# Performance work log

Hardware: AMD Instinct MI355X
Metric: run time of the kernel (lower is better)

## Reference

```python
import jax, jax.numpy as jnp
import numpy as np

N_NODES = 50000
N_EDGES = 600000
CLASSIC_DIM = 128
GRAPH_OUTPUT_DIM = 96
NUM_RELATIONS = 4


def setup_inputs() -> dict:
    key = jax.random.key(0)
    ks = jax.random.split(key, 10)
    x = jax.random.normal(ks[0], (N_NODES, CLASSIC_DIM), dtype=jnp.float32)
    edge_index = jax.random.randint(ks[1], (2, N_EDGES), 0, N_NODES, dtype=jnp.int64)
    edge_type = jax.random.randint(ks[2], (N_EDGES,), 0, NUM_RELATIONS, dtype=jnp.int64)
    s1 = 1.0 / np.sqrt(CLASSIC_DIM)
    W_root1 = jax.random.normal(ks[3], (CLASSIC_DIM, CLASSIC_DIM), dtype=jnp.float32) * s1
    W_rel1 = jax.random.normal(ks[4], (NUM_RELATIONS, CLASSIC_DIM, CLASSIC_DIM), dtype=jnp.float32) * s1
    b1 = jnp.zeros((CLASSIC_DIM,), dtype=jnp.float32)
    W_root2 = jax.random.normal(ks[5], (CLASSIC_DIM, GRAPH_OUTPUT_DIM), dtype=jnp.float32) * s1
    W_rel2 = jax.random.normal(ks[6], (NUM_RELATIONS, CLASSIC_DIM, GRAPH_OUTPUT_DIM), dtype=jnp.float32) * s1
    b2 = jnp.zeros((GRAPH_OUTPUT_DIM,), dtype=jnp.float32)
    return {"classic_features": x, "edge_index": edge_index, "edge_type": edge_type,
            "W_root1": W_root1, "W_rel1": W_rel1, "b1": b1,
            "W_root2": W_root2, "W_rel2": W_rel2, "b2": b2}


def _rgcn_layer(x, edge_index, edge_type, W_root, W_rel, b):
    # RGCN: h_i = W_root x_i + b + sum_r (1/deg_{i,r}) * W_r * sum_{j in N_r(i)} x_j
    # Aggregate-then-transform (valid by linearity) to keep the matmul small.
    src, dst = edge_index[0], edge_index[1]
    msgs = x[src]  # [E, d_in] irregular gather
    out = x @ W_root + b
    n = x.shape[0]
    num_rel = W_rel.shape[0]
    for r in range(num_rel):  # small fixed loop over relation types
        mask = (edge_type == r).astype(x.dtype)  # [E]
        agg = jax.ops.segment_sum(msgs * mask[:, None], dst, num_segments=n)  # [N, d_in]
        deg = jax.ops.segment_sum(mask, dst, num_segments=n)  # [N]
        agg = agg / jnp.maximum(deg, 1.0)[:, None]  # mean per relation (PyG default norm)
        out = out + agg @ W_rel[r]
    return out


def reference(classic_features, edge_index, edge_type, W_root1, W_rel1, b1, W_root2, W_rel2, b2):
    h = _rgcn_layer(classic_features, edge_index, edge_type, W_root1, W_rel1, b1)
    h = jax.nn.relu(h)
    # dropout(0.2) is identity in eval mode
    out = _rgcn_layer(h, edge_index, edge_type, W_root2, W_rel2, b2)
    return out
```

## Files before the change

### kernel.cpp

```cpp
#include <hip/hip_runtime.h>

#define DIM_IN 128
#define NREL 4
#define KTOT (DIM_IN + NREL * DIM_IN)
#define CAP 32

typedef __attribute__((ext_vector_type(8))) short short8;
typedef __attribute__((ext_vector_type(4))) float floatx4;

__device__ inline unsigned short f2bf(float f) {
    union { float f; unsigned int i; } c;
    c.f = f;
    unsigned int r = c.i + 0x7FFF + ((c.i >> 16) & 1);
    return (unsigned short)(r >> 16);
}
__device__ inline float bf2f(unsigned short u) {
    union { unsigned int i; float f; } c;
    c.i = ((unsigned int)u) << 16;
    return c.f;
}

__device__ inline void gload16_lds(const void* g, void* l) {
    __builtin_amdgcn_global_load_lds((const __attribute__((address_space(1))) unsigned int*)g,
                                     (__attribute__((address_space(3))) unsigned int*)l,
                                     16, 0, 0);
}

__global__ __launch_bounds__(256) void prep_kernel(
    const float* __restrict__ x, unsigned short* __restrict__ xb, int n4,
    const float* __restrict__ Wroot1, const float* __restrict__ Wrel1,
    unsigned short* __restrict__ Wt1,
    const float* __restrict__ Wroot2, const float* __restrict__ Wrel2,
    unsigned short* __restrict__ Wt2,
    const int* __restrict__ ei, const int* __restrict__ et,
    int* __restrict__ counts, unsigned short* __restrict__ bucket, int E) {
    int t = blockIdx.x * 256 + threadIdx.x;
    if (t < E) {
        int b = ei[E + t] * NREL + et[t];
        int slot = atomicAdd(&counts[b], 1);
        if (slot < CAP) bucket[(size_t)b * CAP + slot] = (unsigned short)ei[t];
    }
    if (t < n4) {
        float4 v = ((const float4*)x)[t];
        ushort4 o;
        o.x = f2bf(v.x); o.y = f2bf(v.y); o.z = f2bf(v.z); o.w = f2bf(v.w);
        ((ushort4*)xb)[t] = o;
    }
    if (t < 128 * KTOT) {
        int n = t / KTOT, k = t - n * KTOT;
        float v = (k < DIM_IN) ? Wroot1[(size_t)k * 128 + n]
                               : Wrel1[(size_t)(k - DIM_IN) * 128 + n];
        Wt1[t] = f2bf(v);
    }
    if (t < 96 * KTOT) {
        int n = t / KTOT, k = t - n * KTOT;
        float v = (k < DIM_IN) ? Wroot2[(size_t)k * 96 + n]
                               : Wrel2[(size_t)(k - DIM_IN) * 96 + n];
        Wt2[t] = f2bf(v);
    }
}

__global__ __launch_bounds__(256) void agg_kernel(
    const unsigned short* __restrict__ feat, const unsigned short* __restrict__ bucket,
    const int* __restrict__ counts, unsigned short* __restrict__ agg, int nb) {
    int l16 = threadIdx.x & 15;
    int g = (blockIdx.x * 256 + threadIdx.x) >> 4;
    if (g >= nb) return;
    int cnt = counts[g];
    int m = (cnt < CAP) ? cnt : CAP;
    const unsigned short* bk = bucket + (size_t)g * CAP;
    const unsigned short* fb = feat + l16 * 8;
    float acc[8];
#pragma unroll
    for (int j = 0; j < 8; j++) acc[j] = 0.f;
    for (int base = 0; base < m; base += 16) {
        int mm = m - base;
        if (mm > 16) mm = 16;
        int pick = (l16 < mm) ? l16 : (mm - 1);
        int idx = bk[base + pick];
        int s0 = __shfl(idx, 0, 16);
        short8 u = *(const short8*)(fb + (size_t)s0 * DIM_IN);
        for (int j = 1; j < mm; j++) {
            int sn = __shfl(idx, j, 16);
            short8 un = *(const short8*)(fb + (size_t)sn * DIM_IN);
#pragma unroll
            for (int c = 0; c < 8; c++) acc[c] += bf2f((unsigned short)u[c]);
            u = un;
        }
#pragma unroll
        for (int c = 0; c < 8; c++) acc[c] += bf2f((unsigned short)u[c]);
    }
    float sc = (cnt > 0) ? (1.0f / (float)cnt) : 0.f;
    short8 o;
#pragma unroll
    for (int j = 0; j < 8; j++) o[j] = (short)f2bf(acc[j] * sc);
    *(short8*)(agg + (size_t)g * DIM_IN + l16 * 8) = o;
}

template <int NOUT, bool STORE_BF16_RELU>
__global__ __launch_bounds__(256) void mfma_gemm_kernel(
    const unsigned short* __restrict__ xb,
    const unsigned short* __restrict__ agg,
    const unsigned short* __restrict__ Wt,
    const float* __restrict__ bias,
    void* __restrict__ outp,
    int N) {
    constexpr int NT = NOUT / 32;
    constexpr int APAN = 64 * 32;
    constexpr int KS = KTOT / 64;
    __shared__ unsigned short sA[2][2 * APAN];
    const int t = threadIdx.x;
    const int w = t >> 6;
    const int lane = t & 63;
    const int q = lane >> 4;
    const int l15 = lane & 15;
    const int wm = w >> 1, wn = w & 1;
    const int m0 = blockIdx.x * 64;

    floatx4 acc[2][NT];
#pragma unroll
    for (int mt = 0; mt < 2; mt++)
#pragma unroll
        for (int nt = 0; nt < NT; nt++) acc[mt][nt] = (floatx4)0.f;

    const unsigned short* WtB = Wt + (size_t)(wn * (NOUT / 2) + l15) * KTOT + q * 8;

    auto stageA = [&](int ks, int buf) {
        const int k0 = ks * 64;
#pragma unroll
        for (int r = 0; r < 2; r++) {
            int idx = t + r * 256;
            int panel = idx >> 8;
            int rem = idx & 255;
            int row = rem >> 2, ch = rem & 3;
            int rowg = m0 + row;
            if (rowg >= N) rowg = N - 1;
            int col = panel * 32 + ch * 8;
            const unsigned short* gp =
                (k0 < DIM_IN)
                    ? (xb + (size_t)rowg * DIM_IN + k0 + col)
                    : (agg + (size_t)rowg * (NREL * DIM_IN) + (k0 - DIM_IN) + col);
            gload16_lds(gp, &sA[buf][(size_t)idx * 8]);
        }
    };

    stageA(0, 0);
    __syncthreads();
    for (int ks = 0; ks < KS; ks++) {
        const int cur = ks & 1;
        const int k0 = ks * 64;
        short8 bF[2][NT];
#pragma unroll
        for (int s = 0; s < 2; s++)
#pragma unroll
            for (int nt = 0; nt < NT; nt++)
                bF[s][nt] = *(const short8*)(WtB + (size_t)nt * 16 * KTOT + k0 + s * 32);
        if (ks + 1 < KS) stageA(ks + 1, cur ^ 1);
#pragma unroll
        for (int s = 0; s < 2; s++) {
            short8 aF[2];
#pragma unroll
            for (int mt = 0; mt < 2; mt++)
                aF[mt] = *(const short8*)(&sA[cur][(size_t)s * APAN +
                                                   (size_t)(wm * 32 + mt * 16 + l15) * 32 + q * 8]);
#pragma unroll
            for (int mt = 0; mt < 2; mt++)
#pragma unroll
                for (int nt = 0; nt < NT; nt++)
                    acc[mt][nt] = __builtin_amdgcn_mfma_f32_16x16x32_bf16(aF[mt], bF[s][nt],
                                                                          acc[mt][nt], 0, 0, 0);
        }
        __syncthreads();
    }

#pragma unroll
    for (int nt = 0; nt < NT; nt++) {
        int colg = wn * (NOUT / 2) + nt * 16 + l15;
        float bv = bias[colg];
#pragma unroll
        for (int mt = 0; mt < 2; mt++) {
            int rbase = m0 + wm * 32 + mt * 16 + q * 4;
#pragma unroll
            for (int r = 0; r < 4; r++) {
                int grow = rbase + r;
                if (grow < N) {
                    float v = acc[mt][nt][r] + bv;
                    if (STORE_BF16_RELU) {
                        v = fmaxf(v, 0.f);
                        ((unsigned short*)outp)[(size_t)grow * NOUT + colg] = f2bf(v);
                    } else {
                        ((float*)outp)[(size_t)grow * NOUT + colg] = v;
                    }
                }
            }
        }
    }
}

extern "C" void kernel_launch(void* const* d_in, const int* in_sizes, int n_in,
                              void* d_out, int out_size, void* d_ws, size_t ws_size,
                              hipStream_t stream) {
    const float* x = (const float*)d_in[0];
    const int* ei = (const int*)d_in[1];
    const int* et = (const int*)d_in[2];
    const float* Wroot1 = (const float*)d_in[3];
    const float* Wrel1 = (const float*)d_in[4];
    const float* b1 = (const float*)d_in[5];
    const float* Wroot2 = (const float*)d_in[6];
    const float* Wrel2 = (const float*)d_in[7];
    const float* b2 = (const float*)d_in[8];
    float* out = (float*)d_out;

    int N = in_sizes[0] / DIM_IN;
    int E = in_sizes[2];
    int nb = N * NREL;

    char* p = (char*)d_ws;
    unsigned short* xb = (unsigned short*)p;     p += (size_t)N * DIM_IN * 2;
    unsigned short* hb = (unsigned short*)p;     p += (size_t)N * DIM_IN * 2;
    unsigned short* agg = (unsigned short*)p;    p += (size_t)nb * DIM_IN * 2;
    unsigned short* Wt1 = (unsigned short*)p;    p += (size_t)128 * KTOT * 2;
    unsigned short* Wt2 = (unsigned short*)p;    p += (size_t)96 * KTOT * 2;
    int* counts = (int*)p;                       p += (size_t)nb * 4;
    unsigned short* bucket = (unsigned short*)p; p += (size_t)nb * CAP * 2;
    if ((size_t)(p - (char*)d_ws) > ws_size) return;

    int n4 = N * DIM_IN / 4;
    int prepWork = n4;
    if (prepWork < E) prepWork = E;
    if (prepWork < 128 * KTOT) prepWork = 128 * KTOT;

    hipMemsetAsync(counts, 0, (size_t)nb * sizeof(int), stream);
    prep_kernel<<<(prepWork + 255) / 256, 256, 0, stream>>>(
        x, xb, n4, Wroot1, Wrel1, Wt1, Wroot2, Wrel2, Wt2, ei, et, counts, bucket, E);

    int gAgg = (nb * 16 + 255) / 256;
    int gB = (N + 63) / 64;
    agg_kernel<<<gAgg, 256, 0, stream>>>(xb, bucket, counts, agg, nb);
    mfma_gemm_kernel<128, true><<<gB, 256, 0, stream>>>(xb, agg, Wt1, b1, hb, N);
    agg_kernel<<<gAgg, 256, 0, stream>>>(hb, bucket, counts, agg, nb);
    mfma_gemm_kernel<96, false><<<gB, 256, 0, stream>>>(hb, agg, Wt2, b2, out, N);
}
```

Baseline: 266.0 us.

## Fuse neighbor aggregation into GEMM kernel via LDS-resident aggregated tile

Merges the separate aggregation and MFMA GEMM kernels into one kernel per layer. Each 32-row block gathers its neighbors' features, writes the per-relation means straight into a swizzled LDS tile, then runs the GEMM over the full K dimension from LDS with register-prefetched weights. This removes the global agg buffer write and read plus two launches. The cost is smaller GEMM tiles (32 rows), larger LDS use that may lower occupancy, and a serialized gather-then-compute phase inside each block.

```diff
diff --git a/kernel.cpp b/kernel.cpp
--- a/kernel.cpp
+++ b/kernel.cpp
@@ -60,137 +60,140 @@
     }
 }
 
-__global__ __launch_bounds__(256) void agg_kernel(
-    const unsigned short* __restrict__ feat, const unsigned short* __restrict__ bucket,
-    const int* __restrict__ counts, unsigned short* __restrict__ agg, int nb) {
-    int l16 = threadIdx.x & 15;
-    int g = (blockIdx.x * 256 + threadIdx.x) >> 4;
-    if (g >= nb) return;
-    int cnt = counts[g];
-    int m = (cnt < CAP) ? cnt : CAP;
-    const unsigned short* bk = bucket + (size_t)g * CAP;
-    const unsigned short* fb = feat + l16 * 8;
-    float acc[8];
-#pragma unroll
-    for (int j = 0; j < 8; j++) acc[j] = 0.f;
-    for (int base = 0; base < m; base += 16) {
-        int mm = m - base;
-        if (mm > 16) mm = 16;
-        int pick = (l16 < mm) ? l16 : (mm - 1);
-        int idx = bk[base + pick];
-        int s0 = __shfl(idx, 0, 16);
-        short8 u = *(const short8*)(fb + (size_t)s0 * DIM_IN);
-        for (int j = 1; j < mm; j++) {
-            int sn = __shfl(idx, j, 16);
-            short8 un = *(const short8*)(fb + (size_t)sn * DIM_IN);
-#pragma unroll
-            for (int c = 0; c < 8; c++) acc[c] += bf2f((unsigned short)u[c]);
-            u = un;
-        }
-#pragma unroll
-        for (int c = 0; c < 8; c++) acc[c] += bf2f((unsigned short)u[c]);
-    }
-    float sc = (cnt > 0) ? (1.0f / (float)cnt) : 0.f;
-    short8 o;
-#pragma unroll
-    for (int j = 0; j < 8; j++) o[j] = (short)f2bf(acc[j] * sc);
-    *(short8*)(agg + (size_t)g * DIM_IN + l16 * 8) = o;
-}
-
 template <int NOUT, bool STORE_BF16_RELU>
-__global__ __launch_bounds__(256) void mfma_gemm_kernel(
-    const unsigned short* __restrict__ xb,
-    const unsigned short* __restrict__ agg,
+__global__ __launch_bounds__(256) void fused_layer_kernel(
+    const unsigned short* __restrict__ feat,
     const unsigned short* __restrict__ Wt,
     const float* __restrict__ bias,
+    const unsigned short* __restrict__ bucket,
+    const int* __restrict__ counts,
     void* __restrict__ outp,
     int N) {
     constexpr int NT = NOUT / 32;
-    constexpr int APAN = 64 * 32;
-    constexpr int KS = KTOT / 64;
-    __shared__ unsigned short sA[2][2 * APAN];
+    __shared__ unsigned short sA[20 * 32 * 32];
     const int t = threadIdx.x;
     const int w = t >> 6;
     const int lane = t & 63;
     const int q = lane >> 4;
     const int l15 = lane & 15;
+    const int m0 = blockIdx.x * 32;
+
+#pragma unroll
+    for (int i = 0; i < 2; i++) {
+        int slot = i * 256 + t;
+        int p = slot >> 7;
+        int rem = slot & 127;
+        int row = rem >> 2, qs = rem & 3;
+        int qq = qs ^ ((row >> 1) & 3);
+        int rowg = m0 + row;
+        if (rowg >= N) rowg = N - 1;
+        gload16_lds(feat + (size_t)rowg * DIM_IN + p * 32 + qq * 8, sA + (size_t)slot * 8);
+    }
+
+    {
+        int gi = t >> 4, l16 = t & 15;
+        int myBid = gi * 8 + (l16 & 7);
+        int myR = myBid >> 2, myJ = myBid & 3;
+        int myRowg = m0 + myR;
+        if (myRowg >= N) myRowg = N - 1;
+        int cv = counts[myRowg * NREL + myJ];
+        const unsigned short* fb = feat + l16 * 8;
+
+        for (int i = 0; i < 8; i++) {
+            int bid = gi * 8 + i;
+            int r = bid >> 2, j = bid & 3;
+            int rowg = m0 + r;
+            if (rowg >= N) rowg = N - 1;
+            int cnt = __shfl(cv, i, 16);
+            int m = (cnt < CAP) ? cnt : CAP;
+            const unsigned short* bk = bucket + (size_t)(rowg * NREL + j) * CAP;
+            float acc[8];
+#pragma unroll
+            for (int c = 0; c < 8; c++) acc[c] = 0.f;
+            for (int base = 0; base < m; base += 16) {
+                int mm = m - base;
+                if (mm > 16) mm = 16;
+                int pick = (l16 < mm) ? l16 : (mm - 1);
+                int idx = bk[base + pick];
+                int s0 = __shfl(idx, 0, 16);
+                short8 u = *(const short8*)(fb + (size_t)s0 * DIM_IN);
+                for (int jj = 1; jj < mm; jj++) {
+                    int sn = __shfl(idx, jj, 16);
+                    short8 un = *(const short8*)(fb + (size_t)sn * DIM_IN);
+#pragma unroll
+                    for (int c = 0; c < 8; c++) acc[c] += bf2f((unsigned short)u[c]);
+                    u = un;
+                }
+#pragma unroll
+                for (int c = 0; c < 8; c++) acc[c] += bf2f((unsigned short)u[c]);
+            }
+            float sc = (cnt > 0) ? (1.0f / (float)cnt) : 0.f;
+            short8 o;
+#pragma unroll
+            for (int c = 0; c < 8; c++) o[c] = (short)f2bf(acc[c] * sc);
+            int p = 4 + j * 4 + (l16 >> 2);
+            int qs = (l16 & 3) ^ ((r >> 1) & 3);
+            *(short8*)(sA + ((size_t)p * 32 + r) * 32 + qs * 8) = o;
+        }
+    }
+
+    __syncthreads();
+
     const int wm = w >> 1, wn = w & 1;
-    const int m0 = blockIdx.x * 64;
-
-    floatx4 acc[2][NT];
-#pragma unroll
-    for (int mt = 0; mt < 2; mt++)
-#pragma unroll
-        for (int nt = 0; nt < NT; nt++) acc[mt][nt] = (floatx4)0.f;
-
+    floatx4 acc[NT];
+#pragma unroll
+    for (int nt = 0; nt < NT; nt++) acc[nt] = (floatx4)0.f;
+
+    const int rowA = wm * 16 + l15;
+    const int qsA = q ^ ((l15 >> 1) & 3);
+    const unsigned short* sAp = sA + (size_t)rowA * 32 + (size_t)qsA * 8;
     const unsigned short* WtB = Wt + (size_t)(wn * (NOUT / 2) + l15) * KTOT + q * 8;
 
-    auto stageA = [&](int ks, int buf) {
-        const int k0 = ks * 64;
-#pragma unroll
-        for (int r = 0; r < 2; r++) {
-            int idx = t + r * 256;
-            int panel = idx >> 8;
-            int rem = idx & 255;
-            int row = rem >> 2, ch = rem & 3;
-            int rowg = m0 + row;
-            if (rowg >= N) rowg = N - 1;
-            int col = panel * 32 + ch * 8;
-            const unsigned short* gp =
-                (k0 < DIM_IN)
-                    ? (xb + (size_t)rowg * DIM_IN + k0 + col)
-                    : (agg + (size_t)rowg * (NREL * DIM_IN) + (k0 - DIM_IN) + col);
-            gload16_lds(gp, &sA[buf][(size_t)idx * 8]);
-        }
-    };
-
-    stageA(0, 0);
-    __syncthreads();
-    for (int ks = 0; ks < KS; ks++) {
-        const int cur = ks & 1;
-        const int k0 = ks * 64;
-        short8 bF[2][NT];
-#pragma unroll
-        for (int s = 0; s < 2; s++)
+    short8 b0[NT], b1[NT], b0n[NT], b1n[NT];
+#pragma unroll
+    for (int nt = 0; nt < NT; nt++) b0[nt] = *(const short8*)(WtB + (size_t)nt * 16 * KTOT);
+#pragma unroll
+    for (int nt = 0; nt < NT; nt++) b1[nt] = *(const short8*)(WtB + (size_t)nt * 16 * KTOT + 32);
+
+#pragma unroll
+    for (int kp = 0; kp < 10; kp++) {
+        if (kp < 9) {
 #pragma unroll
             for (int nt = 0; nt < NT; nt++)
-                bF[s][nt] = *(const short8*)(WtB + (size_t)nt * 16 * KTOT + k0 + s * 32);
-        if (ks + 1 < KS) stageA(ks + 1, cur ^ 1);
-#pragma unroll
-        for (int s = 0; s < 2; s++) {
-            short8 aF[2];
-#pragma unroll
-            for (int mt = 0; mt < 2; mt++)
-                aF[mt] = *(const short8*)(&sA[cur][(size_t)s * APAN +
-                                                   (size_t)(wm * 32 + mt * 16 + l15) * 32 + q * 8]);
-#pragma unroll
-            for (int mt = 0; mt < 2; mt++)
-#pragma unroll
-                for (int nt = 0; nt < NT; nt++)
-                    acc[mt][nt] = __builtin_amdgcn_mfma_f32_16x16x32_bf16(aF[mt], bF[s][nt],
-                                                                          acc[mt][nt], 0, 0, 0);
-        }
-        __syncthreads();
+                b0n[nt] = *(const short8*)(WtB + (size_t)nt * 16 * KTOT + (2 * kp + 2) * 32);
+        }
+        short8 a0 = *(const short8*)(sAp + (size_t)(2 * kp) * 1024);
+#pragma unroll
+        for (int nt = 0; nt < NT; nt++)
+            acc[nt] = __builtin_amdgcn_mfma_f32_16x16x32_bf16(a0, b0[nt], acc[nt], 0, 0, 0);
+        if (kp < 9) {
+#pragma unroll
+            for (int nt = 0; nt < NT; nt++)
+                b1n[nt] = *(const short8*)(WtB + (size_t)nt * 16 * KTOT + (2 * kp + 3) * 32);
+        }
+        short8 a1 = *(const short8*)(sAp + (size_t)(2 * kp + 1) * 1024);
+#pragma unroll
+        for (int nt = 0; nt < NT; nt++)
+            acc[nt] = __builtin_amdgcn_mfma_f32_16x16x32_bf16(a1, b1[nt], acc[nt], 0, 0, 0);
+#pragma unroll
+        for (int nt = 0; nt < NT; nt++) { b0[nt] = b0n[nt]; b1[nt] = b1n[nt]; }
     }
 
 #pragma unroll
     for (int nt = 0; nt < NT; nt++) {
         int colg = wn * (NOUT / 2) + nt * 16 + l15;
         float bv = bias[colg];
-#pragma unroll
-        for (int mt = 0; mt < 2; mt++) {
-            int rbase = m0 + wm * 32 + mt * 16 + q * 4;
-#pragma unroll
-            for (int r = 0; r < 4; r++) {
-                int grow = rbase + r;
-                if (grow < N) {
-                    float v = acc[mt][nt][r] + bv;
-                    if (STORE_BF16_RELU) {
-                        v = fmaxf(v, 0.f);
-                        ((unsigned short*)outp)[(size_t)grow * NOUT + colg] = f2bf(v);
-                    } else {
-                        ((float*)outp)[(size_t)grow * NOUT + colg] = v;
-                    }
+        int rbase = m0 + wm * 16 + q * 4;
+#pragma unroll
+        for (int r = 0; r < 4; r++) {
+            int grow = rbase + r;
+            if (grow < N) {
+                float v = acc[nt][r] + bv;
+                if (STORE_BF16_RELU) {
+                    v = fmaxf(v, 0.f);
+                    ((unsigned short*)outp)[(size_t)grow * NOUT + colg] = f2bf(v);
+                } else {
+                    ((float*)outp)[(size_t)grow * NOUT + colg] = v;
                 }
             }
         }
@@ -218,7 +221,6 @@
     char* p = (char*)d_ws;
     unsigned short* xb = (unsigned short*)p;     p += (size_t)N * DIM_IN * 2;
     unsigned short* hb = (unsigned short*)p;     p += (size_t)N * DIM_IN * 2;
-    unsigned short* agg = (unsigned short*)p;    p += (size_t)nb * DIM_IN * 2;
     unsigned short* Wt1 = (unsigned short*)p;    p += (size_t)128 * KTOT * 2;
     unsigned short* Wt2 = (unsigned short*)p;    p += (size_t)96 * KTOT * 2;
     int* counts = (int*)p;                       p += (size_t)nb * 4;
@@ -234,10 +236,7 @@
     prep_kernel<<<(prepWork + 255) / 256, 256, 0, stream>>>(
         x, xb, n4, Wroot1, Wrel1, Wt1, Wroot2, Wrel2, Wt2, ei, et, counts, bucket, E);
 
-    int gAgg = (nb * 16 + 255) / 256;
-    int gB = (N + 63) / 64;
-    agg_kernel<<<gAgg, 256, 0, stream>>>(xb, bucket, counts, agg, nb);
-    mfma_gemm_kernel<128, true><<<gB, 256, 0, stream>>>(xb, agg, Wt1, b1, hb, N);
-    agg_kernel<<<gAgg, 256, 0, stream>>>(hb, bucket, counts, agg, nb);
-    mfma_gemm_kernel<96, false><<<gB, 256, 0, stream>>>(hb, agg, Wt2, b2, out, N);
-}
+    int gF = (N + 31) / 32;
+    fused_layer_kernel<128, true><<<gF, 256, 0, stream>>>(xb, Wt1, b1, bucket, counts, hb, N);
+    fused_layer_kernel<96, false><<<gF, 256, 0, stream>>>(hb, Wt2, b2, bucket, counts, out, N);
+}
```

Measured after the change: 326.9 us. 22.9% more time.

## Load full 32-row A tile into LDS once and pipeline B fragments in registers

Applied to the files above, without the earlier changes.

The MFMA GEMM now uses 32-row blocks and stages the entire K=640 A tile into LDS in one pass with an XOR swizzle, instead of double-buffered 64-wide K steps with a sync per step. Weight fragments are prefetched four K-panels ahead in a register ring. This removes the per-step barriers, reduces LDS bank conflicts and doubles the grid size for more parallelism. In exchange it uses more LDS per block, loads weights twice as often per output row and gives each wave half as many MFMAs per A load.

```diff
diff --git a/kernel.cpp b/kernel.cpp
--- a/kernel.cpp
+++ b/kernel.cpp
@@ -106,91 +106,78 @@
     void* __restrict__ outp,
     int N) {
     constexpr int NT = NOUT / 32;
-    constexpr int APAN = 64 * 32;
-    constexpr int KS = KTOT / 64;
-    __shared__ unsigned short sA[2][2 * APAN];
+    __shared__ unsigned short sA[20 * 32 * 32];
     const int t = threadIdx.x;
     const int w = t >> 6;
     const int lane = t & 63;
     const int q = lane >> 4;
     const int l15 = lane & 15;
+    const int m0 = blockIdx.x * 32;
+
+#pragma unroll
+    for (int i = 0; i < 10; i++) {
+        int slot = i * 256 + t;
+        int p = slot >> 7;
+        int rem = slot & 127;
+        int row = rem >> 2, qs = rem & 3;
+        int qq = qs ^ ((row >> 1) & 3);
+        int rowg = m0 + row;
+        if (rowg >= N) rowg = N - 1;
+        const unsigned short* gp =
+            (p < 4) ? (xb + (size_t)rowg * DIM_IN + p * 32 + qq * 8)
+                    : (agg + (size_t)rowg * (NREL * DIM_IN) + (p - 4) * 32 + qq * 8);
+        gload16_lds(gp, sA + (size_t)slot * 8);
+    }
+    __syncthreads();
+
     const int wm = w >> 1, wn = w & 1;
-    const int m0 = blockIdx.x * 64;
-
-    floatx4 acc[2][NT];
-#pragma unroll
-    for (int mt = 0; mt < 2; mt++)
-#pragma unroll
-        for (int nt = 0; nt < NT; nt++) acc[mt][nt] = (floatx4)0.f;
-
+    floatx4 acc[NT];
+#pragma unroll
+    for (int nt = 0; nt < NT; nt++) acc[nt] = (floatx4)0.f;
+
+    const int rowA = wm * 16 + l15;
+    const int qsA = q ^ ((l15 >> 1) & 3);
+    const unsigned short* sAp = sA + (size_t)rowA * 32 + (size_t)qsA * 8;
     const unsigned short* WtB = Wt + (size_t)(wn * (NOUT / 2) + l15) * KTOT + q * 8;
 
-    auto stageA = [&](int ks, int buf) {
-        const int k0 = ks * 64;
-#pragma unroll
-        for (int r = 0; r < 2; r++) {
-            int idx = t + r * 256;
-            int panel = idx >> 8;
-            int rem = idx & 255;
-            int row = rem >> 2, ch = rem & 3;
-            int rowg = m0 + row;
-            if (rowg >= N) rowg = N - 1;
-            int col = panel * 32 + ch * 8;
-            const unsigned short* gp =
-                (k0 < DIM_IN)
-                    ? (xb + (size_t)rowg * DIM_IN + k0 + col)
-                    : (agg + (size_t)rowg * (NREL * DIM_IN) + (k0 - DIM_IN) + col);
-            gload16_lds(gp, &sA[buf][(size_t)idx * 8]);
+    short8 bf[4][NT];
+#pragma unroll
+    for (int d = 0; d < 4; d++)
+#pragma unroll
+        for (int nt = 0; nt < NT; nt++)
+            bf[d][nt] = *(const short8*)(WtB + (size_t)nt * 16 * KTOT + d * 32);
+
+#pragma unroll
+    for (int p = 0; p < 20; p++) {
+        short8 a = *(const short8*)(sAp + (size_t)p * 1024);
+        short8 cur[NT];
+#pragma unroll
+        for (int nt = 0; nt < NT; nt++) cur[nt] = bf[p & 3][nt];
+        if (p + 4 < 20) {
+#pragma unroll
+            for (int nt = 0; nt < NT; nt++)
+                bf[p & 3][nt] = *(const short8*)(WtB + (size_t)nt * 16 * KTOT + (p + 4) * 32);
         }
-    };
-
-    stageA(0, 0);
-    __syncthreads();
-    for (int ks = 0; ks < KS; ks++) {
-        const int cur = ks & 1;
-        const int k0 = ks * 64;
-        short8 bF[2][NT];
-#pragma unroll
-        for (int s = 0; s < 2; s++)
-#pragma unroll
-            for (int nt = 0; nt < NT; nt++)
-                bF[s][nt] = *(const short8*)(WtB + (size_t)nt * 16 * KTOT + k0 + s * 32);
-        if (ks + 1 < KS) stageA(ks + 1, cur ^ 1);
-#pragma unroll
-        for (int s = 0; s < 2; s++) {
-            short8 aF[2];
-#pragma unroll
-            for (int mt = 0; mt < 2; mt++)
-                aF[mt] = *(const short8*)(&sA[cur][(size_t)s * APAN +
-                                                   (size_t)(wm * 32 + mt * 16 + l15) * 32 + q * 8]);
-#pragma unroll
-            for (int mt = 0; mt < 2; mt++)
-#pragma unroll
-                for (int nt = 0; nt < NT; nt++)
-                    acc[mt][nt] = __builtin_amdgcn_mfma_f32_16x16x32_bf16(aF[mt], bF[s][nt],
-                                                                          acc[mt][nt], 0, 0, 0);
-        }
-        __syncthreads();
+#pragma unroll
+        for (int nt = 0; nt < NT; nt++)
+            acc[nt] = __builtin_amdgcn_mfma_f32_16x16x32_bf16(a, cur[nt], acc[nt], 0, 0, 0);
     }
 
 #pragma unroll
     for (int nt = 0; nt < NT; nt++) {
         int colg = wn * (NOUT / 2) + nt * 16 + l15;
         float bv = bias[colg];
-#pragma unroll
-        for (int mt = 0; mt < 2; mt++) {
-            int rbase = m0 + wm * 32 + mt * 16 + q * 4;
-#pragma unroll
-            for (int r = 0; r < 4; r++) {
-                int grow = rbase + r;
-                if (grow < N) {
-                    float v = acc[mt][nt][r] + bv;
-                    if (STORE_BF16_RELU) {
-                        v = fmaxf(v, 0.f);
-                        ((unsigned short*)outp)[(size_t)grow * NOUT + colg] = f2bf(v);
-                    } else {
-                        ((float*)outp)[(size_t)grow * NOUT + colg] = v;
-                    }
+        int rbase = m0 + wm * 16 + q * 4;
+#pragma unroll
+        for (int r = 0; r < 4; r++) {
+            int grow = rbase + r;
+            if (grow < N) {
+                float v = acc[nt][r] + bv;
+                if (STORE_BF16_RELU) {
+                    v = fmaxf(v, 0.f);
+                    ((unsigned short*)outp)[(size_t)grow * NOUT + colg] = f2bf(v);
+                } else {
+                    ((float*)outp)[(size_t)grow * NOUT + colg] = v;
                 }
             }
         }
@@ -235,7 +222,7 @@
         x, xb, n4, Wroot1, Wrel1, Wt1, Wroot2, Wrel2, Wt2, ei, et, counts, bucket, E);
 
     int gAgg = (nb * 16 + 255) / 256;
-    int gB = (N + 63) / 64;
+    int gB = (N + 31) / 32;
     agg_kernel<<<gAgg, 256, 0, stream>>>(xb, bucket, counts, agg, nb);
     mfma_gemm_kernel<128, true><<<gB, 256, 0, stream>>>(xb, agg, Wt1, b1, hb, N);
     agg_kernel<<<gAgg, 256, 0, stream>>>(hb, bucket, counts, agg, nb);
```

Measured after the change: 317.9 us. 1.2x slower.
